# Optimization experiments

Hardware: AMD Instinct MI355X
Metric: run time of the kernel (lower is better)

Reference implementation:

```python
import jax, jax.numpy as jnp
import numpy as np

N_NODES = 50000


def gcn_conv(x, W, b, src, dst, n_nodes):
    """PyG-style GCNConv: self-loops + symmetric deg^-1/2 normalization.

    x: [N, Fin], W: [Fin, Fout], b: [Fout], src/dst: [E] int.
    """
    h = x @ W  # [N, Fout] -- transform before aggregation (small GEMM)
    loop = jnp.arange(n_nodes, dtype=src.dtype)
    src2 = jnp.concatenate([src, loop])  # [E+N]
    dst2 = jnp.concatenate([dst, loop])
    # degree on target nodes (all edge weights = 1, includes self loops)
    deg = jax.ops.segment_sum(jnp.ones(src2.shape[0], dtype=h.dtype), dst2,
                              num_segments=n_nodes)
    dinv = jnp.where(deg > 0, jax.lax.rsqrt(deg), 0.0)
    norm = dinv[src2] * dinv[dst2]  # [E+N]
    msg = h[src2] * norm[:, None]   # gather + scale (memory bound)
    out = jax.ops.segment_sum(msg, dst2, num_segments=n_nodes)  # scatter-add
    return out + b


def setup_inputs() -> dict:
    key = jax.random.key(0)
    ks = jax.random.split(key, 8)
    input_dim, hidden_dim, output_dim = 128, 64, 64
    n_edges = 800000
    x = jax.random.normal(ks[0], (N_NODES, input_dim), dtype=jnp.float32)
    edge_index = jax.random.randint(ks[1], (2, n_edges), 0, N_NODES,
                                    dtype=jnp.int32)
    def glorot(k, fan_in, fan_out):
        s = jnp.sqrt(6.0 / (fan_in + fan_out)).astype(jnp.float32)
        return jax.random.uniform(k, (fan_in, fan_out), jnp.float32, -s, s)
    return {
        "x": x,
        "edge_index": edge_index,
        "W1": glorot(ks[2], input_dim, hidden_dim),
        "b1": jnp.zeros((hidden_dim,), jnp.float32),
        "W2": glorot(ks[3], hidden_dim, output_dim),
        "b2": jnp.zeros((output_dim,), jnp.float32),
        "Wfc": glorot(ks[4], output_dim, 1),
        "bfc": jnp.zeros((1,), jnp.float32),
    }


def reference(x, edge_index, W1, b1, W2, b2, Wfc, bfc):
    src, dst = edge_index[0], edge_index[1]
    h = gcn_conv(x, W1, b1, src, dst, N_NODES)
    h = jax.nn.relu(h)
    h = gcn_conv(h, W2, b2, src, dst, N_NODES)
    logits = h @ Wfc + bfc  # [N, 1]
    return jax.nn.sigmoid(logits)
```

## Files before the change

kernel.cpp:

```cpp
#include <hip/hip_runtime.h>
#include <hip/hip_bf16.h>

#define NN 50000
#define FIN 128
#define FH 64
#define NT (NN / 16)
#define NREG 196
#define RCAP 5120

typedef unsigned short u16;
typedef unsigned int u32;
typedef __attribute__((ext_vector_type(8))) short short8;
typedef __attribute__((ext_vector_type(4))) float floatx4;

__device__ __forceinline__ float b2f(u16 v) {
  union { u32 u; float f; } x; x.u = ((u32)v) << 16; return x.f;
}
__device__ __forceinline__ u16 f2b(float f) {
  union { u32 u; float f; } x; x.f = f;
  u32 r = x.u + 0x7FFFu + ((x.u >> 16) & 1u);
  return (u16)(r >> 16);
}

__global__ __launch_bounds__(256) void k_prep(const u32* __restrict__ xw, int nxw,
                                              const void* __restrict__ w1, int n1w,
                                              const void* __restrict__ w2, int n2w,
                                              const void* __restrict__ wf, int nfw,
                                              const u16* __restrict__ b2,
                                              const u16* __restrict__ bfc,
                                              u16* __restrict__ W1h,
                                              u16* __restrict__ W1l,
                                              float* __restrict__ w2f,
                                              float* __restrict__ cbias,
                                              int* __restrict__ flags,
                                              int* __restrict__ gtail) {
  __shared__ int sc[2];
  int t = threadIdx.x;
  int blk = blockIdx.x;
  if (t < 2) sc[t] = 0;
  __syncthreads();
  if (blk < 32) {
    const u32* p = (const u32*)w1;
    int samples = n1w < 1024 ? n1w : 1024;
    int score = 0;
    for (int i = t; i < samples; i += 256) {
      u32 w = p[i];
      u32 e = (w >> 7) & 0xFFu;
      score += (e >= 100u && e <= 132u) ? 1 : -1;
    }
    if (score) atomicAdd(&sc[0], score);
    if (blk == 0) {
      int sn = nxw < 1024 ? nxw : 1024;
      int sx = 0;
      for (int i = t; i < sn; i += 256) {
        u32 w = xw[i];
        u32 e = (w >> 7) & 0xFFu;
        sx += (e >= 100u && e <= 132u) ? 1 : -1;
      }
      if (sx) atomicAdd(&sc[1], sx);
    }
    __syncthreads();
    int f1 = sc[0] > 0;
    if (blk == 0 && t == 0) {
      flags[0] = sc[1] > 0;
      flags[1] = f1;
      flags[4] = 1;
    }
    int i = blk * 256 + t;
    int j = i & 7, L = (i >> 3) & 63, f = i >> 9;
    int k = (f >> 2) * 32 + (L >> 4) * 8 + j;
    int n = (f & 3) * 16 + (L & 15);
    int idx = k * 64 + n;
    float v = f1 ? b2f(((const u16*)w1)[idx]) : ((const float*)w1)[idx];
    u16 hb = f2b(v);
    W1h[i] = hb;
    W1l[i] = f2b(v - b2f(hb));
  } else {
    for (int i = t; i < NREG; i += 256) gtail[i] = 0;
    const u32* p2 = (const u32*)w2;
    const u32* pf = (const u32*)wf;
    int n2s = n2w < 1024 ? n2w : 1024;
    int nfs = nfw < 1024 ? nfw : 1024;
    int s2 = 0, sf = 0;
    for (int i = t; i < n2s; i += 256) {
      u32 w = p2[i];
      u32 e = (w >> 7) & 0xFFu;
      s2 += (e >= 100u && e <= 132u) ? 1 : -1;
    }
    for (int i = t; i < nfs; i += 256) {
      u32 w = pf[i];
      u32 e = (w >> 7) & 0xFFu;
      sf += (e >= 100u && e <= 132u) ? 1 : -1;
    }
    if (s2) atomicAdd(&sc[0], s2);
    if (sf) atomicAdd(&sc[1], sf);
    __syncthreads();
    int f2 = sc[0] > 0, f3 = sc[1] > 0;
    if (t == 0) { flags[2] = f2; flags[3] = f3; }
    if (t < 64) {
      float acc = 0.f;
      for (int j = 0; j < 64; ++j) {
        float w2v = f2 ? b2f(((const u16*)w2)[t * 64 + j])
                       : ((const float*)w2)[t * 64 + j];
        float wfv = f3 ? b2f(((const u16*)wf)[j]) : ((const float*)wf)[j];
        acc += w2v * wfv;
      }
      w2f[t] = acc;
    } else if (t == 64) {
      float acc = b2f(bfc[0]);
      for (int j = 0; j < 64; ++j) {
        float wfv = f3 ? b2f(((const u16*)wf)[j]) : ((const float*)wf)[j];
        acc += b2f(b2[j]) * wfv;
      }
      cbias[0] = acc;
    }
  }
}

__global__ __launch_bounds__(256) void k_build_gemm(
    const int* __restrict__ src, const int* __restrict__ dst, int E,
    u32* __restrict__ bucket, int* __restrict__ gtail,
    const void* __restrict__ X, const u16* __restrict__ Wh,
    const u16* __restrict__ Wl, u16* __restrict__ out,
    const int* __restrict__ flags) {
  __shared__ int hist[NREG];
  __shared__ int base[NREG];
  int t = threadIdx.x;
  if (blockIdx.x < 256) {
    for (int i = t; i < NREG; i += 256) hist[i] = 0;
    __syncthreads();
    int sl = blockIdx.x, nsl = 256;
    int lo = (int)((long long)sl * E / nsl);
    int hi = (int)((long long)(sl + 1) * E / nsl);
    for (int e = lo + t; e < hi; e += 256) atomicAdd(&hist[dst[e] >> 8], 1);
    __syncthreads();
    for (int i = t; i < NREG; i += 256) {
      int c = hist[i];
      base[i] = (c > 0) ? atomicAdd(&gtail[i], c) : 0;
      hist[i] = 0;
    }
    __syncthreads();
    for (int e = lo + t; e < hi; e += 256) {
      int d = dst[e];
      int r = d >> 8;
      int ofs = base[r] + atomicAdd(&hist[r], 1);
      if (ofs < RCAP)
        bucket[(size_t)r * RCAP + ofs] = ((u32)(d & 255) << 16) | (u32)src[e];
    }
    return;
  }
  constexpr int KC = FIN / 32;
  int wave = t >> 6, lane = t & 63;
  int rt = (blockIdx.x - 256) * 4 + wave;
  if (rt >= NT) return;
  int m = rt * 16 + (lane & 15);
  int q = (lane >> 4) * 8;
  bool xb = flags[0] != 0;

  short8 ah[KC], al[KC];
  if (xb) {
    const u16* xr = (const u16*)X + (size_t)m * FIN + q;
#pragma unroll
    for (int kc = 0; kc < KC; ++kc) ah[kc] = *(const short8*)(xr + kc * 32);
  } else {
    const float* xr = (const float*)X + (size_t)m * FIN + q;
#pragma unroll
    for (int kc = 0; kc < KC; ++kc) {
      float4 v0 = *(const float4*)(xr + kc * 32);
      float4 v1 = *(const float4*)(xr + kc * 32 + 4);
      float v[8] = {v0.x, v0.y, v0.z, v0.w, v1.x, v1.y, v1.z, v1.w};
      short8 h8, l8;
#pragma unroll
      for (int j = 0; j < 8; ++j) {
        u16 hb = f2b(v[j]);
        h8[j] = (short)hb;
        l8[j] = (short)f2b(v[j] - b2f(hb));
      }
      ah[kc] = h8;
      al[kc] = l8;
    }
  }

  int row0 = rt * 16 + (lane >> 4) * 4;
  int c0 = lane & 15;
#pragma unroll
  for (int ct = 0; ct < 4; ++ct) {
    short8 bh[KC], bl[KC];
#pragma unroll
    for (int kc = 0; kc < KC; ++kc) {
      size_t fo = ((size_t)((kc * 4 + ct) * 64 + lane)) * 8;
      bh[kc] = *(const short8*)(Wh + fo);
      bl[kc] = *(const short8*)(Wl + fo);
    }
    floatx4 acc = (floatx4)(0.f);
#pragma unroll
    for (int kc = 0; kc < KC; ++kc) {
      if (!xb)
        acc = __builtin_amdgcn_mfma_f32_16x16x32_bf16(al[kc], bh[kc], acc, 0, 0, 0);
      acc = __builtin_amdgcn_mfma_f32_16x16x32_bf16(ah[kc], bl[kc], acc, 0, 0, 0);
      acc = __builtin_amdgcn_mfma_f32_16x16x32_bf16(ah[kc], bh[kc], acc, 0, 0, 0);
    }
    size_t o = (size_t)row0 * 64 + ct * 16 + c0;
#pragma unroll
    for (int r = 0; r < 4; ++r) out[o + (size_t)r * 64] = f2b(acc[r]);
  }
}

__global__ __launch_bounds__(256) void k_binB1(const u32* __restrict__ bucket,
                                               const int* __restrict__ gtail,
                                               int* __restrict__ cnt,
                                               int* __restrict__ rowstart,
                                               int* __restrict__ bsum,
                                               float* __restrict__ dinv) {
  __shared__ int h[256];
  __shared__ int smem[4];
  int r = blockIdx.x, t = threadIdx.x;
  h[t] = 0;
  __syncthreads();
  int n = gtail[r];
  if (n > RCAP) n = RCAP;
  const u32* b = bucket + (size_t)r * RCAP;
  for (int i = t; i < n; i += 256) atomicAdd(&h[b[i] >> 16], 1);
  __syncthreads();
  int v = r * 256 + t;
  int c = (v < NN) ? h[t] : 0;
  if (v < NN) {
    cnt[v] = c;
    dinv[v] = rsqrtf((float)(c + 1));
  }
  int p = (c + 15) & ~15;
  int lane = t & 63, w = t >> 6;
  int xv = p;
  for (int d = 1; d < 64; d <<= 1) {
    int y = __shfl_up(xv, d);
    if (lane >= d) xv += y;
  }
  if (lane == 63) smem[w] = xv;
  __syncthreads();
  int add = 0;
  for (int j = 0; j < w; ++j) add += smem[j];
  xv += add;
  if (v < NN) rowstart[v] = xv - p;
  if (t == 255) bsum[r] = xv;
}

__global__ __launch_bounds__(256) void k_binB2(const u32* __restrict__ bucket,
                                               const int* __restrict__ gtail,
                                               const int* __restrict__ bsum,
                                               int* __restrict__ rowstart,
                                               const int* __restrict__ cnt,
                                               const float* __restrict__ dinv,
                                               u16* __restrict__ csr,
                                               float* __restrict__ wcsr) {
  __shared__ int off[256];
  __shared__ float dl[256];
  __shared__ int sm[4];
  int r = blockIdx.x, t = threadIdx.x;
  int val = (t < r) ? bsum[t] : 0;
  int lane = t & 63, w = t >> 6;
  for (int o = 32; o > 0; o >>= 1) val += __shfl_xor(val, o);
  if (lane == 0) sm[w] = val;
  __syncthreads();
  int offs = sm[0] + sm[1] + sm[2] + sm[3];
  int v = r * 256 + t;
  int grs = 0;
  if (v < NN) {
    grs = rowstart[v] + offs;
    rowstart[v] = grs;
  }
  off[t] = grs;
  dl[t] = (v < NN) ? dinv[v] : 0.f;
  if (r == NREG - 1 && t == 255) rowstart[NN] = offs + bsum[r];
  __syncthreads();
  int n = gtail[r];
  if (n > RCAP) n = RCAP;
  const u32* b = bucket + (size_t)r * RCAP;
  for (int i = t; i < n; i += 256) {
    u32 p = b[i];
    int local = p >> 16;
    int s = p & 0xFFFFu;
    int pos = atomicAdd(&off[local], 1);
    csr[pos] = (u16)s;
    wcsr[pos] = dinv[s] * dl[local];
  }
  __syncthreads();
  if (v < NN) {
    int end = grs + ((cnt[v] + 15) & ~15);
    for (int pos = off[t]; pos < end; ++pos) {
      csr[pos] = 0;
      wcsr[pos] = 0.f;
    }
  }
}

__global__ __launch_bounds__(256) void k_agg1t(const u16* __restrict__ h,
                                               const float* __restrict__ dinv,
                                               const int* __restrict__ rowstart,
                                               const u16* __restrict__ csr,
                                               const float* __restrict__ wcsr,
                                               const u16* __restrict__ bias,
                                               const float* __restrict__ w2f,
                                               float* __restrict__ t) {
  int tid = threadIdx.x;
  int wave = tid >> 6, lane = tid & 63;
  int v0 = (blockIdx.x * 4 + wave) * 2;
  if (v0 >= NN) return;
  int v1 = v0 + 1;
  float dv0 = dinv[v0], dv1 = dinv[v1];
  float acc0 = b2f(h[(size_t)v0 * 64 + lane]) * (dv0 * dv0);
  float acc1 = b2f(h[(size_t)v1 * 64 + lane]) * (dv1 * dv1);
  int rs0 = rowstart[v0], rsm = rowstart[v1], rse = rowstart[v1 + 1];
  int p0 = rsm - rs0, p1 = rse - rsm;
  int rs1 = rsm;
  int pm = p0 > p1 ? p0 : p1;
  for (int j = 0; j < pm; j += 16) {
    bool a0 = j < p0, a1 = j < p1;
    u32 cw0[8], cw1[8];
    float w0a[16], w1a[16];
    if (a0) {
      int base = rs0 + j;
      uint4 c0 = *(const uint4*)(csr + base);
      uint4 c1 = *(const uint4*)(csr + base + 8);
      cw0[0] = c0.x; cw0[1] = c0.y; cw0[2] = c0.z; cw0[3] = c0.w;
      cw0[4] = c1.x; cw0[5] = c1.y; cw0[6] = c1.z; cw0[7] = c1.w;
      float4 w0 = *(const float4*)(wcsr + base);
      float4 w1 = *(const float4*)(wcsr + base + 4);
      float4 w2 = *(const float4*)(wcsr + base + 8);
      float4 w3 = *(const float4*)(wcsr + base + 12);
      w0a[0]=w0.x; w0a[1]=w0.y; w0a[2]=w0.z; w0a[3]=w0.w;
      w0a[4]=w1.x; w0a[5]=w1.y; w0a[6]=w1.z; w0a[7]=w1.w;
      w0a[8]=w2.x; w0a[9]=w2.y; w0a[10]=w2.z; w0a[11]=w2.w;
      w0a[12]=w3.x; w0a[13]=w3.y; w0a[14]=w3.z; w0a[15]=w3.w;
    }
    if (a1) {
      int base = rs1 + j;
      uint4 c0 = *(const uint4*)(csr + base);
      uint4 c1 = *(const uint4*)(csr + base + 8);
      cw1[0] = c0.x; cw1[1] = c0.y; cw1[2] = c0.z; cw1[3] = c0.w;
      cw1[4] = c1.x; cw1[5] = c1.y; cw1[6] = c1.z; cw1[7] = c1.w;
      float4 w0 = *(const float4*)(wcsr + base);
      float4 w1 = *(const float4*)(wcsr + base + 4);
      float4 w2 = *(const float4*)(wcsr + base + 8);
      float4 w3 = *(const float4*)(wcsr + base + 12);
      w1a[0]=w0.x; w1a[1]=w0.y; w1a[2]=w0.z; w1a[3]=w0.w;
      w1a[4]=w1.x; w1a[5]=w1.y; w1a[6]=w1.z; w1a[7]=w1.w;
      w1a[8]=w2.x; w1a[9]=w2.y; w1a[10]=w2.z; w1a[11]=w2.w;
      w1a[12]=w3.x; w1a[13]=w3.y; w1a[14]=w3.z; w1a[15]=w3.w;
    }
    float hh0[16], hh1[16];
    if (a0) {
#pragma unroll
      for (int i = 0; i < 8; ++i) {
        hh0[2 * i] = b2f(h[(size_t)(cw0[i] & 0xFFFFu) * 64 + lane]);
        hh0[2 * i + 1] = b2f(h[(size_t)(cw0[i] >> 16) * 64 + lane]);
      }
    }
    if (a1) {
#pragma unroll
      for (int i = 0; i < 8; ++i) {
        hh1[2 * i] = b2f(h[(size_t)(cw1[i] & 0xFFFFu) * 64 + lane]);
        hh1[2 * i + 1] = b2f(h[(size_t)(cw1[i] >> 16) * 64 + lane]);
      }
    }
    if (a0) {
#pragma unroll
      for (int i = 0; i < 16; ++i) acc0 += hh0[i] * w0a[i];
    }
    if (a1) {
#pragma unroll
      for (int i = 0; i < 16; ++i) acc1 += hh1[i] * w1a[i];
    }
  }
  float bv = b2f(bias[lane]);
  float wv = w2f[lane];
  float val0 = fmaxf(acc0 + bv, 0.0f) * wv;
  float val1 = fmaxf(acc1 + bv, 0.0f) * wv;
  for (int o = 32; o > 0; o >>= 1) {
    val0 += __shfl_xor(val0, o);
    val1 += __shfl_xor(val1, o);
  }
  if (lane == 0) t[v0] = val0;
  if (lane == 1) t[v1] = val1;
}

__global__ __launch_bounds__(256) void k_aggz(const float* __restrict__ t,
                                              const float* __restrict__ dinv,
                                              const int* __restrict__ rowstart,
                                              const u16* __restrict__ csr,
                                              const float* __restrict__ wcsr,
                                              const float* __restrict__ cbias,
                                              void* __restrict__ out,
                                              const int* __restrict__ flags) {
  int tid = threadIdx.x;
  int wave = tid >> 6, lane = tid & 63;
  int sub = lane >> 4, slot = lane & 15;
  int v = blockIdx.x * 16 + wave * 4 + sub;
  int rs = rowstart[v];
  int pdeg = rowstart[v + 1] - rs;
  float acc = 0.f;
  for (int j = slot; j < pdeg; j += 16) {
    int s = csr[rs + j];
    acc += wcsr[rs + j] * t[s];
  }
  for (int o = 8; o > 0; o >>= 1) acc += __shfl_xor(acc, o);
  if (slot == 0) {
    float dv = dinv[v];
    float z = acc + t[v] * dv * dv + cbias[0];
    float sg = 1.0f / (1.0f + __expf(-z));
    if (flags[0]) ((u16*)out)[v] = f2b(sg);
    else ((float*)out)[v] = sg;
  }
}

extern "C" void kernel_launch(void* const* d_in, const int* in_sizes, int n_in,
                              void* d_out, int out_size, void* d_ws, size_t ws_size,
                              hipStream_t stream) {
  const void* x = d_in[0];
  const int* ei = (const int*)d_in[1];
  const void* W1 = d_in[2];
  const u16* b1 = (const u16*)d_in[3];
  const void* W2 = d_in[4];
  const u16* b2 = (const u16*)d_in[5];
  const void* Wfc = d_in[6];
  const u16* bfc = (const u16*)d_in[7];

  int E = in_sizes[1] / 2;
  const int* src = ei;
  const int* dst = ei + E;

  char* base = (char*)d_ws;
  size_t off = 0;
  auto alloc = [&](size_t bytes) {
    void* p = base + off;
    off = (off + bytes + 255) & ~(size_t)255;
    return p;
  };
  int* flags = (int*)alloc(8 * 4);
  u16* W1h = (u16*)alloc((size_t)FIN * 64 * 2);
  u16* W1l = (u16*)alloc((size_t)FIN * 64 * 2);
  float* w2f = (float*)alloc(64 * 4);
  float* cbias = (float*)alloc(4);
  int* cnt = (int*)alloc((size_t)NN * 4);
  int* rowstart = (int*)alloc((size_t)(NN + 1) * 4);
  int* bsum = (int*)alloc(256 * 4);
  int* gtail = (int*)alloc((size_t)NREG * 4);
  u32* bucket = (u32*)alloc((size_t)NREG * RCAP * 4);
  u16* csr = (u16*)alloc((size_t)(E + 16 * NN) * 2);
  float* wcsr = (float*)alloc((size_t)(E + 16 * NN) * 4);
  float* dinv = (float*)alloc((size_t)NN * 4);
  u16* bufA = (u16*)alloc((size_t)NN * 64 * 2);
  float* tvec = (float*)alloc((size_t)NN * 4);

  k_prep<<<33, 256, 0, stream>>>((const u32*)x, in_sizes[0] / 2, W1,
                                 in_sizes[2] / 2, W2, in_sizes[4] / 2, Wfc,
                                 in_sizes[6] / 2, b2, bfc, W1h, W1l, w2f,
                                 cbias, flags, gtail);
  k_build_gemm<<<256 + (NT + 3) / 4, 256, 0, stream>>>(
      src, dst, E, bucket, gtail, x, W1h, W1l, bufA, flags);
  k_binB1<<<NREG, 256, 0, stream>>>(bucket, gtail, cnt, rowstart, bsum, dinv);
  k_binB2<<<NREG, 256, 0, stream>>>(bucket, gtail, bsum, rowstart, cnt, dinv,
                                    csr, wcsr);
  k_agg1t<<<(NN + 7) / 8, 256, 0, stream>>>(bufA, dinv, rowstart, csr, wcsr,
                                            b1, w2f, tvec);
  k_aggz<<<(NN + 15) / 16, 256, 0, stream>>>(tvec, dinv, rowstart, csr, wcsr,
                                             cbias, d_out, flags);
}
```

Before: 173.1 us.

## Fold degree normalization into features, drop edge weights, restructure kernel pipeline

```diff
diff --git a/kernel.cpp b/kernel.cpp
--- a/kernel.cpp
+++ b/kernel.cpp
@@ -3,10 +3,10 @@
 
 #define NN 50000
 #define FIN 128
-#define FH 64
 #define NT (NN / 16)
 #define NREG 196
 #define RCAP 5120
+#define SLAB 8960
 
 typedef unsigned short u16;
 typedef unsigned int u32;
@@ -22,21 +22,43 @@
   return (u16)(r >> 16);
 }
 
-__global__ __launch_bounds__(256) void k_prep(const u32* __restrict__ xw, int nxw,
-                                              const void* __restrict__ w1, int n1w,
-                                              const void* __restrict__ w2, int n2w,
-                                              const void* __restrict__ wf, int nfw,
-                                              const u16* __restrict__ b2,
-                                              const u16* __restrict__ bfc,
-                                              u16* __restrict__ W1h,
-                                              u16* __restrict__ W1l,
-                                              float* __restrict__ w2f,
-                                              float* __restrict__ cbias,
-                                              int* __restrict__ flags,
-                                              int* __restrict__ gtail) {
-  __shared__ int sc[2];
+__global__ __launch_bounds__(256) void k_prep_binA(
+    const u32* __restrict__ xw, int nxw, const void* __restrict__ w1, int n1w,
+    const void* __restrict__ w2, int n2w, const void* __restrict__ wf, int nfw,
+    const u16* __restrict__ b2, const u16* __restrict__ bfc,
+    u16* __restrict__ W1h, u16* __restrict__ W1l, float* __restrict__ w2f,
+    float* __restrict__ cbias, int* __restrict__ flags,
+    const int* __restrict__ src, const int* __restrict__ dst, int E,
+    u32* __restrict__ bucket, int* __restrict__ gtail,
+    u16* __restrict__ g, float* __restrict__ tvec) {
   int t = threadIdx.x;
   int blk = blockIdx.x;
+  if (blk >= 33) {
+    __shared__ int hist[NREG];
+    __shared__ int base[NREG];
+    for (int i = t; i < NREG; i += 256) hist[i] = 0;
+    __syncthreads();
+    int sl = blk - 33, nsl = 256;
+    int lo = (int)((long long)sl * E / nsl);
+    int hi = (int)((long long)(sl + 1) * E / nsl);
+    for (int e = lo + t; e < hi; e += 256) atomicAdd(&hist[dst[e] >> 8], 1);
+    __syncthreads();
+    for (int i = t; i < NREG; i += 256) {
+      int c = hist[i];
+      base[i] = (c > 0) ? atomicAdd(&gtail[i], c) : 0;
+      hist[i] = 0;
+    }
+    __syncthreads();
+    for (int e = lo + t; e < hi; e += 256) {
+      int d = dst[e];
+      int r = d >> 8;
+      int ofs = base[r] + atomicAdd(&hist[r], 1);
+      if (ofs < RCAP)
+        bucket[(size_t)r * RCAP + ofs] = ((u32)(d & 255) << 16) | (u32)src[e];
+    }
+    return;
+  }
+  __shared__ int sc[2];
   if (t < 2) sc[t] = 0;
   __syncthreads();
   if (blk < 32) {
@@ -64,7 +86,6 @@
     if (blk == 0 && t == 0) {
       flags[0] = sc[1] > 0;
       flags[1] = f1;
-      flags[4] = 1;
     }
     int i = blk * 256 + t;
     int j = i & 7, L = (i >> 3) & 63, f = i >> 9;
@@ -76,7 +97,6 @@
     W1h[i] = hb;
     W1l[i] = f2b(v - b2f(hb));
   } else {
-    for (int i = t; i < NREG; i += 256) gtail[i] = 0;
     const u32* p2 = (const u32*)w2;
     const u32* pf = (const u32*)wf;
     int n2s = n2w < 1024 ? n2w : 1024;
@@ -113,96 +133,11 @@
         acc += b2f(b2[j]) * wfv;
       }
       cbias[0] = acc;
-    }
-  }
-}
-
-__global__ __launch_bounds__(256) void k_build_gemm(
-    const int* __restrict__ src, const int* __restrict__ dst, int E,
-    u32* __restrict__ bucket, int* __restrict__ gtail,
-    const void* __restrict__ X, const u16* __restrict__ Wh,
-    const u16* __restrict__ Wl, u16* __restrict__ out,
-    const int* __restrict__ flags) {
-  __shared__ int hist[NREG];
-  __shared__ int base[NREG];
-  int t = threadIdx.x;
-  if (blockIdx.x < 256) {
-    for (int i = t; i < NREG; i += 256) hist[i] = 0;
-    __syncthreads();
-    int sl = blockIdx.x, nsl = 256;
-    int lo = (int)((long long)sl * E / nsl);
-    int hi = (int)((long long)(sl + 1) * E / nsl);
-    for (int e = lo + t; e < hi; e += 256) atomicAdd(&hist[dst[e] >> 8], 1);
-    __syncthreads();
-    for (int i = t; i < NREG; i += 256) {
-      int c = hist[i];
-      base[i] = (c > 0) ? atomicAdd(&gtail[i], c) : 0;
-      hist[i] = 0;
-    }
-    __syncthreads();
-    for (int e = lo + t; e < hi; e += 256) {
-      int d = dst[e];
-      int r = d >> 8;
-      int ofs = base[r] + atomicAdd(&hist[r], 1);
-      if (ofs < RCAP)
-        bucket[(size_t)r * RCAP + ofs] = ((u32)(d & 255) << 16) | (u32)src[e];
-    }
-    return;
-  }
-  constexpr int KC = FIN / 32;
-  int wave = t >> 6, lane = t & 63;
-  int rt = (blockIdx.x - 256) * 4 + wave;
-  if (rt >= NT) return;
-  int m = rt * 16 + (lane & 15);
-  int q = (lane >> 4) * 8;
-  bool xb = flags[0] != 0;
-
-  short8 ah[KC], al[KC];
-  if (xb) {
-    const u16* xr = (const u16*)X + (size_t)m * FIN + q;
-#pragma unroll
-    for (int kc = 0; kc < KC; ++kc) ah[kc] = *(const short8*)(xr + kc * 32);
-  } else {
-    const float* xr = (const float*)X + (size_t)m * FIN + q;
-#pragma unroll
-    for (int kc = 0; kc < KC; ++kc) {
-      float4 v0 = *(const float4*)(xr + kc * 32);
-      float4 v1 = *(const float4*)(xr + kc * 32 + 4);
-      float v[8] = {v0.x, v0.y, v0.z, v0.w, v1.x, v1.y, v1.z, v1.w};
-      short8 h8, l8;
-#pragma unroll
-      for (int j = 0; j < 8; ++j) {
-        u16 hb = f2b(v[j]);
-        h8[j] = (short)hb;
-        l8[j] = (short)f2b(v[j] - b2f(hb));
-      }
-      ah[kc] = h8;
-      al[kc] = l8;
-    }
-  }
-
-  int row0 = rt * 16 + (lane >> 4) * 4;
-  int c0 = lane & 15;
-#pragma unroll
-  for (int ct = 0; ct < 4; ++ct) {
-    short8 bh[KC], bl[KC];
-#pragma unroll
-    for (int kc = 0; kc < KC; ++kc) {
-      size_t fo = ((size_t)((kc * 4 + ct) * 64 + lane)) * 8;
-      bh[kc] = *(const short8*)(Wh + fo);
-      bl[kc] = *(const short8*)(Wl + fo);
-    }
-    floatx4 acc = (floatx4)(0.f);
-#pragma unroll
-    for (int kc = 0; kc < KC; ++kc) {
-      if (!xb)
-        acc = __builtin_amdgcn_mfma_f32_16x16x32_bf16(al[kc], bh[kc], acc, 0, 0, 0);
-      acc = __builtin_amdgcn_mfma_f32_16x16x32_bf16(ah[kc], bl[kc], acc, 0, 0, 0);
-      acc = __builtin_amdgcn_mfma_f32_16x16x32_bf16(ah[kc], bh[kc], acc, 0, 0, 0);
-    }
-    size_t o = (size_t)row0 * 64 + ct * 16 + c0;
-#pragma unroll
-    for (int r = 0; r < 4; ++r) out[o + (size_t)r * 64] = f2b(acc[r]);
+    } else if (t >= 128 && t < 192) {
+      g[(size_t)NN * 64 + (t - 128)] = 0;
+    } else if (t == 192) {
+      tvec[NN] = 0.f;
+    }
   }
 }
 
@@ -210,7 +145,6 @@
                                                const int* __restrict__ gtail,
                                                int* __restrict__ cnt,
                                                int* __restrict__ rowstart,
-                                               int* __restrict__ bsum,
                                                float* __restrict__ dinv) {
   __shared__ int h[256];
   __shared__ int smem[4];
@@ -240,154 +174,175 @@
   int add = 0;
   for (int j = 0; j < w; ++j) add += smem[j];
   xv += add;
-  if (v < NN) rowstart[v] = xv - p;
-  if (t == 255) bsum[r] = xv;
-}
-
-__global__ __launch_bounds__(256) void k_binB2(const u32* __restrict__ bucket,
-                                               const int* __restrict__ gtail,
-                                               const int* __restrict__ bsum,
-                                               int* __restrict__ rowstart,
-                                               const int* __restrict__ cnt,
-                                               const float* __restrict__ dinv,
-                                               u16* __restrict__ csr,
-                                               float* __restrict__ wcsr) {
-  __shared__ int off[256];
-  __shared__ float dl[256];
-  __shared__ int sm[4];
-  int r = blockIdx.x, t = threadIdx.x;
-  int val = (t < r) ? bsum[t] : 0;
-  int lane = t & 63, w = t >> 6;
-  for (int o = 32; o > 0; o >>= 1) val += __shfl_xor(val, o);
-  if (lane == 0) sm[w] = val;
-  __syncthreads();
-  int offs = sm[0] + sm[1] + sm[2] + sm[3];
-  int v = r * 256 + t;
-  int grs = 0;
-  if (v < NN) {
-    grs = rowstart[v] + offs;
-    rowstart[v] = grs;
-  }
-  off[t] = grs;
-  dl[t] = (v < NN) ? dinv[v] : 0.f;
-  if (r == NREG - 1 && t == 255) rowstart[NN] = offs + bsum[r];
-  __syncthreads();
-  int n = gtail[r];
-  if (n > RCAP) n = RCAP;
-  const u32* b = bucket + (size_t)r * RCAP;
-  for (int i = t; i < n; i += 256) {
-    u32 p = b[i];
-    int local = p >> 16;
-    int s = p & 0xFFFFu;
-    int pos = atomicAdd(&off[local], 1);
-    csr[pos] = (u16)s;
-    wcsr[pos] = dinv[s] * dl[local];
-  }
-  __syncthreads();
-  if (v < NN) {
-    int end = grs + ((cnt[v] + 15) & ~15);
-    for (int pos = off[t]; pos < end; ++pos) {
-      csr[pos] = 0;
-      wcsr[pos] = 0.f;
-    }
-  }
-}
-
-__global__ __launch_bounds__(256) void k_agg1t(const u16* __restrict__ h,
+  if (v < NN) rowstart[v] = r * SLAB + xv - p;
+}
+
+__global__ __launch_bounds__(256) void k_gemm_scatter(
+    const u32* __restrict__ bucket, const int* __restrict__ gtail,
+    const int* __restrict__ rowstart, const int* __restrict__ cnt,
+    u16* __restrict__ csr,
+    const void* __restrict__ X, const u16* __restrict__ Wh,
+    const u16* __restrict__ Wl, const float* __restrict__ dinv,
+    u16* __restrict__ g, const int* __restrict__ flags) {
+  int t = threadIdx.x;
+  if (blockIdx.x < NREG) {
+    __shared__ int off[256];
+    int r = blockIdx.x;
+    int v = r * 256 + t;
+    int grs = (v < NN) ? rowstart[v] : 0;
+    off[t] = grs;
+    __syncthreads();
+    int n = gtail[r];
+    if (n > RCAP) n = RCAP;
+    const u32* b = bucket + (size_t)r * RCAP;
+    for (int i = t; i < n; i += 256) {
+      u32 p = b[i];
+      int pos = atomicAdd(&off[p >> 16], 1);
+      csr[pos] = (u16)(p & 0xFFFFu);
+    }
+    __syncthreads();
+    if (v < NN) {
+      int end = grs + ((cnt[v] + 15) & ~15);
+      for (int pos = off[t]; pos < end; ++pos) csr[pos] = (u16)NN;
+    }
+    return;
+  }
+  constexpr int KC = FIN / 32;
+  int wave = t >> 6, lane = t & 63;
+  int rt = (blockIdx.x - NREG) * 4 + wave;
+  if (rt >= NT) return;
+  int m = rt * 16 + (lane & 15);
+  int q = (lane >> 4) * 8;
+  bool xb = flags[0] != 0;
+
+  short8 ah[KC], al[KC];
+  if (xb) {
+    const u16* xr = (const u16*)X + (size_t)m * FIN + q;
+#pragma unroll
+    for (int kc = 0; kc < KC; ++kc) ah[kc] = *(const short8*)(xr + kc * 32);
+  } else {
+    const float* xr = (const float*)X + (size_t)m * FIN + q;
+#pragma unroll
+    for (int kc = 0; kc < KC; ++kc) {
+      float4 v0 = *(const float4*)(xr + kc * 32);
+      float4 v1 = *(const float4*)(xr + kc * 32 + 4);
+      float v[8] = {v0.x, v0.y, v0.z, v0.w, v1.x, v1.y, v1.z, v1.w};
+      short8 h8, l8;
+#pragma unroll
+      for (int j = 0; j < 8; ++j) {
+        u16 hb = f2b(v[j]);
+        h8[j] = (short)hb;
+        l8[j] = (short)f2b(v[j] - b2f(hb));
+      }
+      ah[kc] = h8;
+      al[kc] = l8;
+    }
+  }
+
+  int row0 = rt * 16 + (lane >> 4) * 4;
+  int c0 = lane & 15;
+  float dvr[4];
+#pragma unroll
+  for (int r = 0; r < 4; ++r) dvr[r] = dinv[row0 + r];
+#pragma unroll
+  for (int ct = 0; ct < 4; ++ct) {
+    short8 bh[KC], bl[KC];
+#pragma unroll
+    for (int kc = 0; kc < KC; ++kc) {
+      size_t fo = ((size_t)((kc * 4 + ct) * 64 + lane)) * 8;
+      bh[kc] = *(const short8*)(Wh + fo);
+      bl[kc] = *(const short8*)(Wl + fo);
+    }
+    floatx4 acc = (floatx4)(0.f);
+#pragma unroll
+    for (int kc = 0; kc < KC; ++kc) {
+      if (!xb)
+        acc = __builtin_amdgcn_mfma_f32_16x16x32_bf16(al[kc], bh[kc], acc, 0, 0, 0);
+      acc = __builtin_amdgcn_mfma_f32_16x16x32_bf16(ah[kc], bl[kc], acc, 0, 0, 0);
+      acc = __builtin_amdgcn_mfma_f32_16x16x32_bf16(ah[kc], bh[kc], acc, 0, 0, 0);
+    }
+    size_t o = (size_t)row0 * 64 + ct * 16 + c0;
+#pragma unroll
+    for (int r = 0; r < 4; ++r) g[o + (size_t)r * 64] = f2b(acc[r] * dvr[r]);
+  }
+}
+
+__global__ __launch_bounds__(256) void k_agg1t(const u16* __restrict__ g,
                                                const float* __restrict__ dinv,
                                                const int* __restrict__ rowstart,
+                                               const int* __restrict__ cnt,
                                                const u16* __restrict__ csr,
-                                               const float* __restrict__ wcsr,
                                                const u16* __restrict__ bias,
                                                const float* __restrict__ w2f,
-                                               float* __restrict__ t) {
+                                               float* __restrict__ tvec) {
   int tid = threadIdx.x;
   int wave = tid >> 6, lane = tid & 63;
-  int v0 = (blockIdx.x * 4 + wave) * 2;
-  if (v0 >= NN) return;
-  int v1 = v0 + 1;
-  float dv0 = dinv[v0], dv1 = dinv[v1];
-  float acc0 = b2f(h[(size_t)v0 * 64 + lane]) * (dv0 * dv0);
-  float acc1 = b2f(h[(size_t)v1 * 64 + lane]) * (dv1 * dv1);
-  int rs0 = rowstart[v0], rsm = rowstart[v1], rse = rowstart[v1 + 1];
-  int p0 = rsm - rs0, p1 = rse - rsm;
-  int rs1 = rsm;
-  int pm = p0 > p1 ? p0 : p1;
+  int v = (blockIdx.x * 4 + wave) * 4;
+  int rs[4], pd[4];
+  float dvl[4], acc[4];
+  int pm = 0;
+#pragma unroll
+  for (int n = 0; n < 4; ++n) {
+    rs[n] = rowstart[v + n];
+    pd[n] = (cnt[v + n] + 15) & ~15;
+    dvl[n] = dinv[v + n];
+    acc[n] = b2f(g[(size_t)(v + n) * 64 + lane]);
+    pm = pd[n] > pm ? pd[n] : pm;
+  }
   for (int j = 0; j < pm; j += 16) {
-    bool a0 = j < p0, a1 = j < p1;
-    u32 cw0[8], cw1[8];
-    float w0a[16], w1a[16];
-    if (a0) {
-      int base = rs0 + j;
-      uint4 c0 = *(const uint4*)(csr + base);
-      uint4 c1 = *(const uint4*)(csr + base + 8);
-      cw0[0] = c0.x; cw0[1] = c0.y; cw0[2] = c0.z; cw0[3] = c0.w;
-      cw0[4] = c1.x; cw0[5] = c1.y; cw0[6] = c1.z; cw0[7] = c1.w;
-      float4 w0 = *(const float4*)(wcsr + base);
-      float4 w1 = *(const float4*)(wcsr + base + 4);
-      float4 w2 = *(const float4*)(wcsr + base + 8);
-      float4 w3 = *(const float4*)(wcsr + base + 12);
-      w0a[0]=w0.x; w0a[1]=w0.y; w0a[2]=w0.z; w0a[3]=w0.w;
-      w0a[4]=w1.x; w0a[5]=w1.y; w0a[6]=w1.z; w0a[7]=w1.w;
-      w0a[8]=w2.x; w0a[9]=w2.y; w0a[10]=w2.z; w0a[11]=w2.w;
-      w0a[12]=w3.x; w0a[13]=w3.y; w0a[14]=w3.z; w0a[15]=w3.w;
-    }
-    if (a1) {
-      int base = rs1 + j;
-      uint4 c0 = *(const uint4*)(csr + base);
-      uint4 c1 = *(const uint4*)(csr + base + 8);
-      cw1[0] = c0.x; cw1[1] = c0.y; cw1[2] = c0.z; cw1[3] = c0.w;
-      cw1[4] = c1.x; cw1[5] = c1.y; cw1[6] = c1.z; cw1[7] = c1.w;
-      float4 w0 = *(const float4*)(wcsr + base);
-      float4 w1 = *(const float4*)(wcsr + base + 4);
-      float4 w2 = *(const float4*)(wcsr + base + 8);
-      float4 w3 = *(const float4*)(wcsr + base + 12);
-      w1a[0]=w0.x; w1a[1]=w0.y; w1a[2]=w0.z; w1a[3]=w0.w;
-      w1a[4]=w1.x; w1a[5]=w1.y; w1a[6]=w1.z; w1a[7]=w1.w;
-      w1a[8]=w2.x; w1a[9]=w2.y; w1a[10]=w2.z; w1a[11]=w2.w;
-      w1a[12]=w3.x; w1a[13]=w3.y; w1a[14]=w3.z; w1a[15]=w3.w;
-    }
-    float hh0[16], hh1[16];
-    if (a0) {
-#pragma unroll
-      for (int i = 0; i < 8; ++i) {
-        hh0[2 * i] = b2f(h[(size_t)(cw0[i] & 0xFFFFu) * 64 + lane]);
-        hh0[2 * i + 1] = b2f(h[(size_t)(cw0[i] >> 16) * 64 + lane]);
-      }
-    }
-    if (a1) {
-#pragma unroll
-      for (int i = 0; i < 8; ++i) {
-        hh1[2 * i] = b2f(h[(size_t)(cw1[i] & 0xFFFFu) * 64 + lane]);
-        hh1[2 * i + 1] = b2f(h[(size_t)(cw1[i] >> 16) * 64 + lane]);
-      }
-    }
-    if (a0) {
-#pragma unroll
-      for (int i = 0; i < 16; ++i) acc0 += hh0[i] * w0a[i];
-    }
-    if (a1) {
-#pragma unroll
-      for (int i = 0; i < 16; ++i) acc1 += hh1[i] * w1a[i];
+    u32 cw[4][8];
+    bool act[4];
+#pragma unroll
+    for (int n = 0; n < 4; ++n) {
+      act[n] = j < pd[n];
+      if (act[n]) {
+        int b = rs[n] + j;
+        uint4 c0 = *(const uint4*)(csr + b);
+        uint4 c1 = *(const uint4*)(csr + b + 8);
+        cw[n][0] = c0.x; cw[n][1] = c0.y; cw[n][2] = c0.z; cw[n][3] = c0.w;
+        cw[n][4] = c1.x; cw[n][5] = c1.y; cw[n][6] = c1.z; cw[n][7] = c1.w;
+      }
+    }
+    float hh[4][16];
+#pragma unroll
+    for (int n = 0; n < 4; ++n) {
+      if (act[n]) {
+#pragma unroll
+        for (int i = 0; i < 8; ++i) {
+          hh[n][2 * i] = b2f(g[(size_t)(cw[n][i] & 0xFFFFu) * 64 + lane]);
+          hh[n][2 * i + 1] = b2f(g[(size_t)(cw[n][i] >> 16) * 64 + lane]);
+        }
+      }
+    }
+#pragma unroll
+    for (int n = 0; n < 4; ++n) {
+      if (act[n]) {
+        float s0 = (hh[n][0] + hh[n][1]) + (hh[n][2] + hh[n][3]);
+        float s1 = (hh[n][4] + hh[n][5]) + (hh[n][6] + hh[n][7]);
+        float s2 = (hh[n][8] + hh[n][9]) + (hh[n][10] + hh[n][11]);
+        float s3 = (hh[n][12] + hh[n][13]) + (hh[n][14] + hh[n][15]);
+        acc[n] += (s0 + s1) + (s2 + s3);
+      }
     }
   }
   float bv = b2f(bias[lane]);
-  float wv = w2f[lane];
-  float val0 = fmaxf(acc0 + bv, 0.0f) * wv;
-  float val1 = fmaxf(acc1 + bv, 0.0f) * wv;
-  for (int o = 32; o > 0; o >>= 1) {
-    val0 += __shfl_xor(val0, o);
-    val1 += __shfl_xor(val1, o);
-  }
-  if (lane == 0) t[v0] = val0;
-  if (lane == 1) t[v1] = val1;
-}
-
-__global__ __launch_bounds__(256) void k_aggz(const float* __restrict__ t,
+  float wfv = w2f[lane];
+  float val[4];
+#pragma unroll
+  for (int n = 0; n < 4; ++n) {
+    val[n] = fmaxf(dvl[n] * acc[n] + bv, 0.0f) * wfv;
+    for (int o = 32; o > 0; o >>= 1) val[n] += __shfl_xor(val[n], o);
+  }
+#pragma unroll
+  for (int n = 0; n < 4; ++n)
+    if (lane == n) tvec[v + n] = dvl[n] * val[n];
+}
+
+__global__ __launch_bounds__(256) void k_aggz(const float* __restrict__ tvec,
                                               const float* __restrict__ dinv,
                                               const int* __restrict__ rowstart,
+                                              const int* __restrict__ cnt,
                                               const u16* __restrict__ csr,
-                                              const float* __restrict__ wcsr,
                                               const float* __restrict__ cbias,
                                               void* __restrict__ out,
                                               const int* __restrict__ flags) {
@@ -396,16 +351,13 @@
   int sub = lane >> 4, slot = lane & 15;
   int v = blockIdx.x * 16 + wave * 4 + sub;
   int rs = rowstart[v];
-  int pdeg = rowstart[v + 1] - rs;
+  int pdeg = (cnt[v] + 15) & ~15;
   float acc = 0.f;
-  for (int j = slot; j < pdeg; j += 16) {
-    int s = csr[rs + j];
-    acc += wcsr[rs + j] * t[s];
-  }
+  for (int j = slot; j < pdeg; j += 16) acc += tvec[csr[rs + j]];
   for (int o = 8; o > 0; o >>= 1) acc += __shfl_xor(acc, o);
   if (slot == 0) {
     float dv = dinv[v];
-    float z = acc + t[v] * dv * dv + cbias[0];
+    float z = dv * (acc + tvec[v]) + cbias[0];
     float sg = 1.0f / (1.0f + __expf(-z));
     if (flags[0]) ((u16*)out)[v] = f2b(sg);
     else ((float*)out)[v] = sg;
@@ -441,27 +393,24 @@
   float* w2f = (float*)alloc(64 * 4);
   float* cbias = (float*)alloc(4);
   int* cnt = (int*)alloc((size_t)NN * 4);
-  int* rowstart = (int*)alloc((size_t)(NN + 1) * 4);
-  int* bsum = (int*)alloc(256 * 4);
+  int* rowstart = (int*)alloc((size_t)NN * 4);
   int* gtail = (int*)alloc((size_t)NREG * 4);
   u32* bucket = (u32*)alloc((size_t)NREG * RCAP * 4);
-  u16* csr = (u16*)alloc((size_t)(E + 16 * NN) * 2);
-  float* wcsr = (float*)alloc((size_t)(E + 16 * NN) * 4);
+  u16* csr = (u16*)alloc((size_t)NREG * SLAB * 2);
   float* dinv = (float*)alloc((size_t)NN * 4);
-  u16* bufA = (u16*)alloc((size_t)NN * 64 * 2);
-  float* tvec = (float*)alloc((size_t)NN * 4);
-
-  k_prep<<<33, 256, 0, stream>>>((const u32*)x, in_sizes[0] / 2, W1,
-                                 in_sizes[2] / 2, W2, in_sizes[4] / 2, Wfc,
-                                 in_sizes[6] / 2, b2, bfc, W1h, W1l, w2f,
-                                 cbias, flags, gtail);
-  k_build_gemm<<<256 + (NT + 3) / 4, 256, 0, stream>>>(
-      src, dst, E, bucket, gtail, x, W1h, W1l, bufA, flags);
-  k_binB1<<<NREG, 256, 0, stream>>>(bucket, gtail, cnt, rowstart, bsum, dinv);
-  k_binB2<<<NREG, 256, 0, stream>>>(bucket, gtail, bsum, rowstart, cnt, dinv,
-                                    csr, wcsr);
-  k_agg1t<<<(NN + 7) / 8, 256, 0, stream>>>(bufA, dinv, rowstart, csr, wcsr,
-                                            b1, w2f, tvec);
-  k_aggz<<<(NN + 15) / 16, 256, 0, stream>>>(tvec, dinv, rowstart, csr, wcsr,
-                                             cbias, d_out, flags);
-}
+  u16* g = (u16*)alloc((size_t)(NN + 1) * 64 * 2);
+  float* tvec = (float*)alloc((size_t)(NN + 1) * 4);
+
+  hipMemsetAsync(gtail, 0, (size_t)NREG * 4, stream);
+  k_prep_binA<<<289, 256, 0, stream>>>(
+      (const u32*)x, in_sizes[0] / 2, W1, in_sizes[2] / 2, W2, in_sizes[4] / 2,
+      Wfc, in_sizes[6] / 2, b2, bfc, W1h, W1l, w2f, cbias, flags, src, dst, E,
+      bucket, gtail, g, tvec);
+  k_binB1<<<NREG, 256, 0, stream>>>(bucket, gtail, cnt, rowstart, dinv);
+  k_gemm_scatter<<<NREG + (NT + 3) / 4, 256, 0, stream>>>(
+      bucket, gtail, rowstart, cnt, csr, x, W1h, W1l, dinv, g, flags);
+  k_agg1t<<<NN / 16, 256, 0, stream>>>(g, dinv, rowstart, cnt, csr, b1, w2f,
+                                       tvec);
+  k_aggz<<<NN / 16, 256, 0, stream>>>(tvec, dinv, rowstart, cnt, csr, cbias,
+                                      d_out, flags);
+}
```

New measurement: 158.3 us (median of 2 runs). -8.6%, faster.
